# Kernel optimization log

Hardware: AMD Instinct MI355X
Metric: run time of the kernel (lower is better)

## Reference

```python
import jax, jax.numpy as jnp
import numpy as np


def _conv1x1(x, w, b):
    # x: [B,C,H,W], w: [O,C], b: [O] -> [B,O,H,W]
    return jnp.einsum('bchw,oc->bohw', x, w) + b[None, :, None, None]


def _maxpool2x2(x):
    # MaxPool2d(kernel_size=2, stride=2), VALID padding
    return jax.lax.reduce_window(
        x, -jnp.inf, jax.lax.max,
        window_dimensions=(1, 1, 2, 2),
        window_strides=(1, 1, 2, 2),
        padding='VALID')


def setup_inputs() -> dict:
    key = jax.random.key(0)
    ks = jax.random.split(key, 9)
    B, C, H, W = 8, 256, 64, 64
    c = 128  # in_channels // channel_scale_factor
    s = 0.05
    return {
        'x': jax.random.normal(ks[0], (B, C, H, W), jnp.float32),
        'theta_w': jax.random.normal(ks[1], (c, C), jnp.float32) * s,
        'theta_b': jax.random.normal(ks[2], (c,), jnp.float32) * s,
        'phi_w': jax.random.normal(ks[3], (c, C), jnp.float32) * s,
        'phi_b': jax.random.normal(ks[4], (c,), jnp.float32) * s,
        'g_w': jax.random.normal(ks[5], (c, C), jnp.float32) * s,
        'g_b': jax.random.normal(ks[6], (c,), jnp.float32) * s,
        'wz_w': jax.random.normal(ks[7], (C, c), jnp.float32) * s,
        'wz_b': jax.random.normal(ks[8], (C,), jnp.float32) * s,
    }


def reference(x, theta_w, theta_b, phi_w, phi_b, g_w, g_b, wz_w, wz_b):
    B, C, H, W = x.shape
    c = theta_w.shape[0]
    ox = x
    theta = _conv1x1(x, theta_w, theta_b)              # [B,c,H,W]
    xp = _maxpool2x2(x)                                # [B,C,h,w]
    phi = _conv1x1(xp, phi_w, phi_b)                   # [B,c,h,w]
    gi = _conv1x1(xp, g_w, g_b)                        # [B,c,h,w]

    N = H * W
    M = phi.shape[2] * phi.shape[3]
    theta1 = theta.reshape(B, c, N).transpose(0, 2, 1)  # [B,N,c]
    phi1 = phi.reshape(B, c, M)                         # [B,c,M]
    gi1 = gi.reshape(B, c, M).transpose(0, 2, 1)        # [B,M,c]

    m1 = jnp.einsum('bnc,bcm->bnm', theta1, phi1)       # [B,N,M] attention scores
    m1 = jax.nn.softmax(m1, axis=2)
    m2 = jnp.einsum('bnm,bmc->bnc', m1, gi1)            # [B,N,c]
    # Faithful to torch .view: raw-buffer reinterpretation, no transpose
    m3 = m2.reshape(B, c, H, W)
    m4 = _conv1x1(m3, wz_w, wz_b)                       # [B,C,H,W]
    return m4 + ox
```

## Files before the change

### kernel.cpp

```cpp
#include <hip/hip_runtime.h>
#include <math.h>

#define BATCH 8
#define CINCH 256
#define CMID  128
#define NPIX  4096
#define MPIX  1024

typedef __attribute__((ext_vector_type(8))) short bf16x8;
typedef __attribute__((ext_vector_type(4))) short s16x4;
typedef __attribute__((ext_vector_type(4))) float f32x4;

static __device__ __forceinline__ short f2bf(float f) {
    unsigned u = __float_as_uint(f);
    u = (u + 0x7fffu + ((u >> 16) & 1u)) >> 16;
    return (short)u;
}
static __device__ __forceinline__ float bf2f(short s) {
    return __uint_as_float(((unsigned)(unsigned short)s) << 16);
}

static __device__ __forceinline__ void gl16(const void* g, void* l) {
    __builtin_amdgcn_global_load_lds(
        (const __attribute__((address_space(1))) void*)g,
        (__attribute__((address_space(3))) void*)l, 16, 0, 0);
}

__global__ __launch_bounds__(256)
void wcvt_k(const float* __restrict__ a, const float* __restrict__ b,
            const float* __restrict__ c, const float* __restrict__ d,
            short* __restrict__ o)
{
    int i = (blockIdx.x * 256 + threadIdx.x) * 4;
    if (i < 32768) {
        int cr = i >> 8, col = i & 255;
        int R = (cr & 7) * 16 + (cr >> 3);
        float4 v = *(const float4*)(a + i);
        s16x4 rv = { f2bf(v.x * 1.44269504f), f2bf(v.y * 1.44269504f),
                     f2bf(v.z * 1.44269504f), f2bf(v.w * 1.44269504f) };
        *(s16x4*)(o + R * 256 + col) = rv;
    } else {
        const float* src; int j;
        if (i < 65536)      { src = b; j = i - 32768; }
        else if (i < 98304) { src = c; j = i - 65536; }
        else                { src = d; j = i - 98304; }
        float4 v = *(const float4*)(src + j);
        s16x4 rv = { f2bf(v.x), f2bf(v.y), f2bf(v.z), f2bf(v.w) };
        *(s16x4*)(o + i) = rv;
    }
}

__global__ __launch_bounds__(1024)
void front_k(const float* __restrict__ x,
             const short* __restrict__ th_wh, const float* __restrict__ th_b,
             const short* __restrict__ ph_wh, const float* __restrict__ ph_b,
             const short* __restrict__ g_wh,  const float* __restrict__ g_b,
             short* __restrict__ thetaO, short* __restrict__ phiO,
             short* __restrict__ gO)
{
    __shared__ float F[128 * 65];
    __shared__ short X[128 * 264];
    __shared__ short P[32 * 264];

    const int bid = blockIdx.x;
    const int t   = threadIdx.x;
    const int b   = bid & 7;
    const int r   = bid >> 3;
    const int wv  = t >> 6;
    const int l   = t & 63;
    const int lr  = l & 15;
    const int lg  = l >> 4;

    const int hh = wv & 1;
    const int c0 = wv >> 1;
    float ra[8], rb[8];
    {
        const float* xb = x + ((size_t)(b * 256)) * 4096 + r * 128;
#pragma unroll
        for (int i = 0; i < 8; ++i)
            ra[i] = xb[(size_t)(c0 + i * 8) * 4096 + hh * 64 + l];
    }
#pragma unroll
    for (int ct = 0; ct < 4; ++ct) {
        if ((ct & 1) == 0) {
#pragma unroll
            for (int i = 0; i < 8; ++i) F[(hh * 64 + l) * 65 + c0 + i * 8] = ra[i];
            if (ct < 3) {
                const float* xb = x + ((size_t)(b * 256 + (ct + 1) * 64)) * 4096 + r * 128;
#pragma unroll
                for (int i = 0; i < 8; ++i)
                    rb[i] = xb[(size_t)(c0 + i * 8) * 4096 + hh * 64 + l];
            }
        } else {
#pragma unroll
            for (int i = 0; i < 8; ++i) F[(hh * 64 + l) * 65 + c0 + i * 8] = rb[i];
            if (ct < 3) {
                const float* xb = x + ((size_t)(b * 256 + (ct + 1) * 64)) * 4096 + r * 128;
#pragma unroll
                for (int i = 0; i < 8; ++i)
                    ra[i] = xb[(size_t)(c0 + i * 8) * 4096 + hh * 64 + l];
            }
        }
        asm volatile("s_waitcnt lgkmcnt(0)" ::: "memory");
        __builtin_amdgcn_s_barrier();
#pragma unroll
        for (int i = 0; i < 8; ++i) {
            int slot = i * 1024 + t;
            int row = slot >> 6, ch = slot & 63;
            X[row * 264 + ct * 64 + ch] = f2bf(F[row * 65 + ch]);
        }
        asm volatile("s_waitcnt lgkmcnt(0)" ::: "memory");
        __builtin_amdgcn_s_barrier();
    }

#pragma unroll
    for (int i = 0; i < 2; ++i) {
        int slot = i * 1024 + t;
        int wp = slot >> 6, c4 = slot & 63;
        s16x4 v0 = *(const s16x4*)(X + (2 * wp) * 264 + c4 * 4);
        s16x4 v1 = *(const s16x4*)(X + (2 * wp + 1) * 264 + c4 * 4);
        s16x4 v2 = *(const s16x4*)(X + (64 + 2 * wp) * 264 + c4 * 4);
        s16x4 v3 = *(const s16x4*)(X + (65 + 2 * wp) * 264 + c4 * 4);
        s16x4 rm;
#pragma unroll
        for (int e = 0; e < 4; ++e) {
            float m = fmaxf(fmaxf(bf2f(v0[e]), bf2f(v1[e])),
                            fmaxf(bf2f(v2[e]), bf2f(v3[e])));
            rm[e] = f2bf(m);
        }
        *(s16x4*)(P + wp * 264 + c4 * 4) = rm;
    }
    __syncthreads();

    if (wv < 8) {
        const int m0 = wv * 16;
        f32x4 o[8];
#pragma unroll
        for (int dt = 0; dt < 8; ++dt)
#pragma unroll
            for (int e = 0; e < 4; ++e) o[dt][e] = 0.f;
        for (int kt = 0; kt < 8; ++kt) {
            bf16x8 a = *(const bf16x8*)(X + (m0 + lr) * 264 + kt * 32 + lg * 8);
#pragma unroll
            for (int dt = 0; dt < 8; ++dt) {
                bf16x8 bv = *(const bf16x8*)(th_wh + (size_t)(dt * 16 + lr) * 256 + kt * 32 + lg * 8);
                o[dt] = __builtin_amdgcn_mfma_f32_16x16x32_bf16(a, bv, o[dt], 0, 0, 0);
            }
        }
        float bvt[8];
#pragma unroll
        for (int dt = 0; dt < 8; ++dt) bvt[dt] = th_b[lr * 8 + dt] * 1.44269504f;
        short* ob = thetaO + (size_t)b * NPIX * 128;
#pragma unroll
        for (int rr = 0; rr < 4; ++rr) {
            int n = r * 128 + m0 + lg * 4 + rr;
            bf16x8 sv;
#pragma unroll
            for (int dt = 0; dt < 8; ++dt) sv[dt] = f2bf(o[dt][rr] + bvt[dt]);
            *(bf16x8*)(ob + (size_t)n * 128 + lr * 8) = sv;
        }
    } else {
        const int j    = wv & 3;
        const int half = j & 1;
        const int coH  = j >> 1;
        const bool isPhi = (wv < 12);
        const short* wsel = (isPhi ? ph_wh : g_wh) + (size_t)coH * 64 * 256;
        const float* bsel = isPhi ? ph_b : g_b;

        f32x4 q[4];
#pragma unroll
        for (int dt = 0; dt < 4; ++dt)
#pragma unroll
            for (int e = 0; e < 4; ++e) q[dt][e] = 0.f;
        for (int kt = 0; kt < 8; ++kt) {
            bf16x8 a = *(const bf16x8*)(P + (half * 16 + lr) * 264 + kt * 32 + lg * 8);
#pragma unroll
            for (int dt = 0; dt < 4; ++dt) {
                bf16x8 bv = *(const bf16x8*)(wsel + (size_t)(dt * 16 + lr) * 256 + kt * 32 + lg * 8);
                q[dt] = __builtin_amdgcn_mfma_f32_16x16x32_bf16(a, bv, q[dt], 0, 0, 0);
            }
        }
        float bv4[4];
#pragma unroll
        for (int dt = 0; dt < 4; ++dt) bv4[dt] = bsel[coH * 64 + dt * 16 + lr];

        if (isPhi) {
            short* cb = phiO + (size_t)b * 32 * 4096 + (size_t)r * 4096;
#pragma unroll
            for (int rr = 0; rr < 4; ++rr) {
                int mloc = half * 16 + lg * 4 + rr;
                short* cbb = cb + (mloc >> 4) * 512 + (mloc & 15) * 8;
#pragma unroll
                for (int dt = 0; dt < 4; ++dt) {
                    int cc = coH * 64 + dt * 16 + lr;
                    cbb[(cc >> 5) * 1024 + ((cc >> 3) & 3) * 128 + (cc & 7)]
                        = f2bf(q[dt][rr] + bv4[dt]);
                }
            }
        } else {
            short* cb = gO + (size_t)b * 32 * 4096 + (size_t)r * 4096;
            const int keyblk = half * 2 + (lg >> 1);
#pragma unroll
            for (int dt = 0; dt < 4; ++dt) {
                int cc = coH * 64 + dt * 16 + lr;
                s16x4 sv;
#pragma unroll
                for (int rr = 0; rr < 4; ++rr) sv[rr] = f2bf(q[dt][rr] + bv4[dt]);
                *(s16x4*)(cb + (size_t)((cc >> 4) * 64 + keyblk * 16 + (cc & 15)) * 8
                             + (lg & 1) * 4) = sv;
            }
        }
    }
}

__global__ __launch_bounds__(512)
void attn_fz(const short* __restrict__ theta, const short* __restrict__ phi_sw,
             const short* __restrict__ G_sw, const short* __restrict__ wzh,
             const float* __restrict__ wzb, const float* __restrict__ x,
             float* __restrict__ out)
{
    __shared__ __align__(16) char smem[147456];
    const int t   = threadIdx.x;
    const int wv  = t >> 6;
    const int l   = t & 63;
    const int lr  = l & 15;
    const int lg  = l >> 4;
    const int gid = wv >> 2;
    const int wvl = wv & 3;
    const int bid = blockIdx.x;
    const int b   = bid & 7;
    const int s   = bid >> 3;

    const short* thb = theta + (size_t)b * NPIX * 128;
    const char*  phC = (const char*)phi_sw + (size_t)b * 32 * 8192;
    const char*  gC  = (const char*)G_sw  + (size_t)b * 32 * 8192;
    const int first = gid * 16;

    auto STAGEP = [&](int bufi, int pi) {
#pragma unroll
        for (int sub = 0; sub < 2; ++sub) {
            int chunk = first + pi * 2 + sub;
            const char* ps = phC + (size_t)chunk * 8192 + wvl * 2048 + l * 16;
            const char* gs = gC  + (size_t)chunk * 8192 + wvl * 2048 + l * 16;
            char* base = smem + gid * 65536 + bufi * 32768 + sub * 16384;
            gl16(ps,        base + wvl * 2048);
            gl16(ps + 1024, base + wvl * 2048 + 1024);
            gl16(gs,        base + 8192 + wvl * 2048);
            gl16(gs + 1024, base + 8192 + wvl * 2048 + 1024);
        }
    };

    STAGEP(0, 0);

    bf16x8 bq[2][4];
#pragma unroll
    for (int u = 0; u < 2; ++u) {
        int n = ((wvl * 2 + u) * 16 + lr) * 32 + s;
#pragma unroll
        for (int kt = 0; kt < 4; ++kt)
            bq[u][kt] = *(const bf16x8*)(thb + (size_t)n * 128 + kt * 32 + lg * 8);
    }

    f32x4 o[2][8];
#pragma unroll
    for (int u = 0; u < 2; ++u)
#pragma unroll
        for (int dt = 0; dt < 8; ++dt)
#pragma unroll
            for (int e = 0; e < 4; ++e) o[u][dt][e] = 0.f;
    float ps_[2] = { 0.f, 0.f };

    for (int pi = 0; pi < 8; ++pi) {
        asm volatile("s_waitcnt vmcnt(0)" ::: "memory");
        __builtin_amdgcn_s_barrier();
        if (pi < 7) STAGEP((pi + 1) & 1, pi + 1);

#pragma unroll
        for (int sub = 0; sub < 2; ++sub) {
            const short* pb = (const short*)(smem + gid * 65536 + (pi & 1) * 32768
                                             + sub * 16384);
            const short* gb = pb + 4096;

            f32x4 ssw[2][2];
#pragma unroll
            for (int u = 0; u < 2; ++u)
#pragma unroll
                for (int mt = 0; mt < 2; ++mt)
#pragma unroll
                    for (int e = 0; e < 4; ++e) ssw[u][mt][e] = 0.f;
#pragma unroll
            for (int kt = 0; kt < 4; ++kt) {
                bf16x8 a0 = *(const bf16x8*)(pb + ((kt * 2 + 0) * 64 + l) * 8);
                bf16x8 a1 = *(const bf16x8*)(pb + ((kt * 2 + 1) * 64 + l) * 8);
#pragma unroll
                for (int u = 0; u < 2; ++u) {
                    ssw[u][0] = __builtin_amdgcn_mfma_f32_16x16x32_bf16(a0, bq[u][kt], ssw[u][0], 0, 0, 0);
                    ssw[u][1] = __builtin_amdgcn_mfma_f32_16x16x32_bf16(a1, bq[u][kt], ssw[u][1], 0, 0, 0);
                }
            }

            bf16x8 gf[8];
#pragma unroll
            for (int dt = 0; dt < 8; ++dt)
                gf[dt] = *(const bf16x8*)(gb + (dt * 64 + l) * 8);

#pragma unroll
            for (int u = 0; u < 2; ++u) {
                short* pu = (short*)(smem + 131072 + wv * 2048 + u * 1024);
#pragma unroll
                for (int mt = 0; mt < 2; ++mt) {
                    s16x4 pv;
#pragma unroll
                    for (int rr = 0; rr < 4; ++rr) {
                        float p = exp2f(ssw[u][mt][rr] - 40.f);
                        ps_[u] += p;
                        pv[rr] = f2bf(p);
                    }
                    *(s16x4*)(pu + ((mt * 2 + (lg >> 1)) * 16 + lr) * 8 + (lg & 1) * 4) = pv;
                }
                bf16x8 pa = *(const bf16x8*)(pu + l * 8);
#pragma unroll
                for (int dt = 0; dt < 8; ++dt)
                    o[u][dt] = __builtin_amdgcn_mfma_f32_16x16x32_bf16(pa, gf[dt], o[u][dt], 0, 0, 0);
            }
        }
    }

    const int co0 = wv * 32;
    bf16x8 afr[2][4];
#pragma unroll
    for (int nt = 0; nt < 2; ++nt) {
        int co = co0 + nt * 16 + lr;
#pragma unroll
        for (int kt = 0; kt < 4; ++kt)
            afr[nt][kt] = *(const bf16x8*)(wzh + (size_t)co * 128 + kt * 32 + lg * 8);
    }

    __syncthreads();
    float* mg = (float*)smem;
    short* m3l = (short*)(smem + 73728);
    if (wv >= 4) {
        float* mb = mg + (size_t)((wv - 4) * 64 + l) * 68;
#pragma unroll
        for (int u = 0; u < 2; ++u)
#pragma unroll
            for (int dt = 0; dt < 8; ++dt)
                *(f32x4*)(mb + (u * 8 + dt) * 4) = o[u][dt];
        mb[64] = ps_[0]; mb[65] = ps_[1];
    }
    __syncthreads();
    if (wv < 4) {
        const float* mb = mg + (size_t)(wv * 64 + l) * 68;
#pragma unroll
        for (int u = 0; u < 2; ++u)
#pragma unroll
            for (int dt = 0; dt < 8; ++dt) {
                f32x4 pv = *(const f32x4*)(mb + (u * 8 + dt) * 4);
#pragma unroll
                for (int e = 0; e < 4; ++e) o[u][dt][e] += pv[e];
            }
        ps_[0] += mb[64]; ps_[1] += mb[65];

#pragma unroll
        for (int u = 0; u < 2; ++u) {
            float tot = ps_[u];
            tot += __shfl_xor(tot, 16);
            tot += __shfl_xor(tot, 32);
            float inv = 1.f / tot;
            float invg[4];
#pragma unroll
            for (int rr = 0; rr < 4; ++rr) invg[rr] = __shfl(inv, lg * 4 + rr);
            const int cmb = (wvl * 2 + u) * 2 + (lg >> 1);
#pragma unroll
            for (int dt = 0; dt < 8; ++dt) {
                s16x4 zv;
#pragma unroll
                for (int rr = 0; rr < 4; ++rr) zv[rr] = f2bf(o[u][dt][rr] * invg[rr]);
                *(s16x4*)(m3l + (size_t)(cmb * 128 + dt * 16 + lr) * 8 + (lg & 1) * 4) = zv;
            }
        }
    }
    __syncthreads();

    {
        float xr[2][4][8];
#pragma unroll
        for (int nt = 0; nt < 2; ++nt)
#pragma unroll
            for (int rr = 0; rr < 4; ++rr) {
                int co = co0 + nt * 16 + lg * 4 + rr;
                const float* xb = x + ((size_t)b * 256 + co) * 4096 + s * 128;
#pragma unroll
                for (int dt = 0; dt < 8; ++dt)
                    xr[nt][rr][dt] = xb[dt * 16 + lr];
            }

        f32x4 oc[2][8];
#pragma unroll
        for (int nt = 0; nt < 2; ++nt)
#pragma unroll
            for (int dt = 0; dt < 8; ++dt)
#pragma unroll
                for (int e = 0; e < 4; ++e) oc[nt][dt][e] = 0.f;

#pragma unroll
        for (int dt = 0; dt < 8; ++dt) {
#pragma unroll
            for (int kt = 0; kt < 4; ++kt) {
                bf16x8 bz = *(const bf16x8*)(m3l + (size_t)((kt * 4 + lg) * 128 + dt * 16 + lr) * 8);
                oc[0][dt] = __builtin_amdgcn_mfma_f32_16x16x32_bf16(afr[0][kt], bz, oc[0][dt], 0, 0, 0);
                oc[1][dt] = __builtin_amdgcn_mfma_f32_16x16x32_bf16(afr[1][kt], bz, oc[1][dt], 0, 0, 0);
            }
        }

#pragma unroll
        for (int nt = 0; nt < 2; ++nt)
#pragma unroll
            for (int rr = 0; rr < 4; ++rr) {
                int co = co0 + nt * 16 + lg * 4 + rr;
                float bv = wzb[co];
                float* ob = out + ((size_t)b * 256 + co) * 4096 + s * 128;
#pragma unroll
                for (int dt = 0; dt < 8; ++dt) {
                    int lp = dt * 16 + lr;
                    ob[lp] = oc[nt][dt][rr] + bv + xr[nt][rr][dt];
                }
            }
    }
}

extern "C" void kernel_launch(void* const* d_in, const int* in_sizes, int n_in,
                              void* d_out, int out_size, void* d_ws, size_t ws_size,
                              hipStream_t stream)
{
    const float* x       = (const float*)d_in[0];
    const float* theta_w = (const float*)d_in[1];
    const float* theta_b = (const float*)d_in[2];
    const float* phi_w   = (const float*)d_in[3];
    const float* phi_b   = (const float*)d_in[4];
    const float* g_w     = (const float*)d_in[5];
    const float* g_b     = (const float*)d_in[6];
    const float* wz_w    = (const float*)d_in[7];
    const float* wz_b    = (const float*)d_in[8];
    float* out = (float*)d_out;

    short* ws      = (short*)d_ws;
    short* theta_h = ws;
    short* phi_h   = theta_h + (size_t)4194304;
    short* G_h     = phi_h + (size_t)1048576;
    short* wh      = G_h  + (size_t)1048576;
    short* th_wh = wh;
    short* ph_wh = wh + 32768;
    short* g_wh  = wh + 65536;
    short* wz_wh = wh + 98304;

    wcvt_k<<<dim3(128), 256, 0, stream>>>(theta_w, phi_w, g_w, wz_w, wh);

    front_k<<<dim3(256), 1024, 0, stream>>>(x, th_wh, theta_b, ph_wh, phi_b,
                                            g_wh, g_b, theta_h, phi_h, G_h);

    attn_fz<<<dim3(256), 512, 0, stream>>>(theta_h, phi_h, G_h,
                                           wz_wh, wz_b, x, out);
}
```

Measured before the change: 74.48 us.

## Double waves per attention block and use triple-buffered single-chunk staging

```diff
diff --git a/kernel.cpp b/kernel.cpp
--- a/kernel.cpp
+++ b/kernel.cpp
@@ -213,20 +213,20 @@
     }
 }
 
-__global__ __launch_bounds__(512)
+__global__ __launch_bounds__(1024, 4)
 void attn_fz(const short* __restrict__ theta, const short* __restrict__ phi_sw,
              const short* __restrict__ G_sw, const short* __restrict__ wzh,
              const float* __restrict__ wzb, const float* __restrict__ x,
              float* __restrict__ out)
 {
-    __shared__ __align__(16) char smem[147456];
+    __shared__ __align__(16) char smem[114688];
     const int t   = threadIdx.x;
     const int wv  = t >> 6;
     const int l   = t & 63;
     const int lr  = l & 15;
     const int lg  = l >> 4;
-    const int gid = wv >> 2;
-    const int wvl = wv & 3;
+    const int gid = wv >> 3;
+    const int wvl = wv & 7;
     const int bid = blockIdx.x;
     const int b   = bid & 7;
     const int s   = bid >> 3;
@@ -236,196 +236,160 @@
     const char*  gC  = (const char*)G_sw  + (size_t)b * 32 * 8192;
     const int first = gid * 16;
 
-    auto STAGEP = [&](int bufi, int pi) {
-#pragma unroll
-        for (int sub = 0; sub < 2; ++sub) {
-            int chunk = first + pi * 2 + sub;
-            const char* ps = phC + (size_t)chunk * 8192 + wvl * 2048 + l * 16;
-            const char* gs = gC  + (size_t)chunk * 8192 + wvl * 2048 + l * 16;
-            char* base = smem + gid * 65536 + bufi * 32768 + sub * 16384;
-            gl16(ps,        base + wvl * 2048);
-            gl16(ps + 1024, base + wvl * 2048 + 1024);
-            gl16(gs,        base + 8192 + wvl * 2048);
-            gl16(gs + 1024, base + 8192 + wvl * 2048 + 1024);
-        }
+    auto STAGE = [&](int bufi, int cc) {
+        int chunk = first + cc;
+        const char* ps = phC + (size_t)chunk * 8192 + wvl * 1024 + l * 16;
+        const char* gs = gC  + (size_t)chunk * 8192 + wvl * 1024 + l * 16;
+        char* base = smem + (gid * 3 + bufi) * 16384;
+        gl16(ps, base + wvl * 1024);
+        gl16(gs, base + 8192 + wvl * 1024);
     };
 
-    STAGEP(0, 0);
-
-    bf16x8 bq[2][4];
-#pragma unroll
-    for (int u = 0; u < 2; ++u) {
-        int n = ((wvl * 2 + u) * 16 + lr) * 32 + s;
+    STAGE(0, 0);
+    STAGE(1, 1);
+
+    bf16x8 bq[4];
+    {
+        int n = (wvl * 16 + lr) * 32 + s;
 #pragma unroll
         for (int kt = 0; kt < 4; ++kt)
-            bq[u][kt] = *(const bf16x8*)(thb + (size_t)n * 128 + kt * 32 + lg * 8);
-    }
-
-    f32x4 o[2][8];
-#pragma unroll
-    for (int u = 0; u < 2; ++u)
+            bq[kt] = *(const bf16x8*)(thb + (size_t)n * 128 + kt * 32 + lg * 8);
+    }
+
+    f32x4 o[8];
+#pragma unroll
+    for (int dt = 0; dt < 8; ++dt)
+#pragma unroll
+        for (int e = 0; e < 4; ++e) o[dt][e] = 0.f;
+    float ps_ = 0.f;
+
+    for (int c = 0; c < 16; ++c) {
+        if (c < 15) asm volatile("s_waitcnt vmcnt(2)" ::: "memory");
+        else        asm volatile("s_waitcnt vmcnt(0)" ::: "memory");
+        __builtin_amdgcn_s_barrier();
+        if (c < 14) STAGE((c + 2) % 3, c + 2);
+
+        const short* pb = (const short*)(smem + (gid * 3 + c % 3) * 16384);
+        const short* gb = pb + 4096;
+
+        f32x4 ssw[2];
+#pragma unroll
+        for (int mt = 0; mt < 2; ++mt)
+#pragma unroll
+            for (int e = 0; e < 4; ++e) ssw[mt][e] = 0.f;
+#pragma unroll
+        for (int kt = 0; kt < 4; ++kt) {
+            bf16x8 a0 = *(const bf16x8*)(pb + ((kt * 2 + 0) * 64 + l) * 8);
+            bf16x8 a1 = *(const bf16x8*)(pb + ((kt * 2 + 1) * 64 + l) * 8);
+            ssw[0] = __builtin_amdgcn_mfma_f32_16x16x32_bf16(a0, bq[kt], ssw[0], 0, 0, 0);
+            ssw[1] = __builtin_amdgcn_mfma_f32_16x16x32_bf16(a1, bq[kt], ssw[1], 0, 0, 0);
+        }
+
+        bf16x8 gf[8];
 #pragma unroll
         for (int dt = 0; dt < 8; ++dt)
-#pragma unroll
-            for (int e = 0; e < 4; ++e) o[u][dt][e] = 0.f;
-    float ps_[2] = { 0.f, 0.f };
-
-    for (int pi = 0; pi < 8; ++pi) {
-        asm volatile("s_waitcnt vmcnt(0)" ::: "memory");
-        __builtin_amdgcn_s_barrier();
-        if (pi < 7) STAGEP((pi + 1) & 1, pi + 1);
-
-#pragma unroll
-        for (int sub = 0; sub < 2; ++sub) {
-            const short* pb = (const short*)(smem + gid * 65536 + (pi & 1) * 32768
-                                             + sub * 16384);
-            const short* gb = pb + 4096;
-
-            f32x4 ssw[2][2];
-#pragma unroll
-            for (int u = 0; u < 2; ++u)
-#pragma unroll
-                for (int mt = 0; mt < 2; ++mt)
-#pragma unroll
-                    for (int e = 0; e < 4; ++e) ssw[u][mt][e] = 0.f;
-#pragma unroll
-            for (int kt = 0; kt < 4; ++kt) {
-                bf16x8 a0 = *(const bf16x8*)(pb + ((kt * 2 + 0) * 64 + l) * 8);
-                bf16x8 a1 = *(const bf16x8*)(pb + ((kt * 2 + 1) * 64 + l) * 8);
-#pragma unroll
-                for (int u = 0; u < 2; ++u) {
-                    ssw[u][0] = __builtin_amdgcn_mfma_f32_16x16x32_bf16(a0, bq[u][kt], ssw[u][0], 0, 0, 0);
-                    ssw[u][1] = __builtin_amdgcn_mfma_f32_16x16x32_bf16(a1, bq[u][kt], ssw[u][1], 0, 0, 0);
-                }
-            }
-
-            bf16x8 gf[8];
-#pragma unroll
-            for (int dt = 0; dt < 8; ++dt)
-                gf[dt] = *(const bf16x8*)(gb + (dt * 64 + l) * 8);
-
-#pragma unroll
-            for (int u = 0; u < 2; ++u) {
-                short* pu = (short*)(smem + 131072 + wv * 2048 + u * 1024);
-#pragma unroll
-                for (int mt = 0; mt < 2; ++mt) {
-                    s16x4 pv;
-#pragma unroll
-                    for (int rr = 0; rr < 4; ++rr) {
-                        float p = exp2f(ssw[u][mt][rr] - 40.f);
-                        ps_[u] += p;
-                        pv[rr] = f2bf(p);
-                    }
-                    *(s16x4*)(pu + ((mt * 2 + (lg >> 1)) * 16 + lr) * 8 + (lg & 1) * 4) = pv;
-                }
-                bf16x8 pa = *(const bf16x8*)(pu + l * 8);
-#pragma unroll
-                for (int dt = 0; dt < 8; ++dt)
-                    o[u][dt] = __builtin_amdgcn_mfma_f32_16x16x32_bf16(pa, gf[dt], o[u][dt], 0, 0, 0);
-            }
-        }
-    }
-
-    const int co0 = wv * 32;
-    bf16x8 afr[2][4];
-#pragma unroll
-    for (int nt = 0; nt < 2; ++nt) {
-        int co = co0 + nt * 16 + lr;
-#pragma unroll
-        for (int kt = 0; kt < 4; ++kt)
-            afr[nt][kt] = *(const bf16x8*)(wzh + (size_t)co * 128 + kt * 32 + lg * 8);
-    }
+            gf[dt] = *(const bf16x8*)(gb + (dt * 64 + l) * 8);
+
+        short* pu = (short*)(smem + 98304) + wv * 512;
+#pragma unroll
+        for (int mt = 0; mt < 2; ++mt) {
+            s16x4 pv;
+#pragma unroll
+            for (int rr = 0; rr < 4; ++rr) {
+                float p = exp2f(ssw[mt][rr] - 40.f);
+                ps_ += p;
+                pv[rr] = f2bf(p);
+            }
+            *(s16x4*)(pu + ((mt * 2 + (lg >> 1)) * 16 + lr) * 8 + (lg & 1) * 4) = pv;
+        }
+        bf16x8 pa = *(const bf16x8*)(pu + l * 8);
+#pragma unroll
+        for (int dt = 0; dt < 8; ++dt)
+            o[dt] = __builtin_amdgcn_mfma_f32_16x16x32_bf16(pa, gf[dt], o[dt], 0, 0, 0);
+    }
+
+    const int co0 = wv * 16;
+    bf16x8 afr[4];
+#pragma unroll
+    for (int kt = 0; kt < 4; ++kt)
+        afr[kt] = *(const bf16x8*)(wzh + (size_t)(co0 + lr) * 128 + kt * 32 + lg * 8);
 
     __syncthreads();
     float* mg = (float*)smem;
     short* m3l = (short*)(smem + 73728);
-    if (wv >= 4) {
-        float* mb = mg + (size_t)((wv - 4) * 64 + l) * 68;
-#pragma unroll
-        for (int u = 0; u < 2; ++u)
+    if (wv >= 8) {
+        float* mb = mg + (size_t)((wv - 8) * 64 + l) * 33;
+#pragma unroll
+        for (int dt = 0; dt < 8; ++dt)
+            *(f32x4*)(mb + dt * 4) = o[dt];
+        mb[32] = ps_;
+    }
+    __syncthreads();
+    if (wv < 8) {
+        const float* mb = mg + (size_t)(wv * 64 + l) * 33;
+#pragma unroll
+        for (int dt = 0; dt < 8; ++dt) {
+            f32x4 pv = *(const f32x4*)(mb + dt * 4);
+#pragma unroll
+            for (int e = 0; e < 4; ++e) o[dt][e] += pv[e];
+        }
+        ps_ += mb[32];
+
+        float tot = ps_;
+        tot += __shfl_xor(tot, 16);
+        tot += __shfl_xor(tot, 32);
+        float inv = 1.f / tot;
+        float invg[4];
+#pragma unroll
+        for (int rr = 0; rr < 4; ++rr) invg[rr] = __shfl(inv, lg * 4 + rr);
+        const int cmb = wvl * 2 + (lg >> 1);
+#pragma unroll
+        for (int dt = 0; dt < 8; ++dt) {
+            s16x4 zv;
+#pragma unroll
+            for (int rr = 0; rr < 4; ++rr) zv[rr] = f2bf(o[dt][rr] * invg[rr]);
+            *(s16x4*)(m3l + (size_t)(cmb * 128 + dt * 16 + lr) * 8 + (lg & 1) * 4) = zv;
+        }
+    }
+    __syncthreads();
+
+    {
+        float xr[4][8];
+#pragma unroll
+        for (int rr = 0; rr < 4; ++rr) {
+            int co = co0 + lg * 4 + rr;
+            const float* xb = x + ((size_t)b * 256 + co) * 4096 + s * 128;
 #pragma unroll
             for (int dt = 0; dt < 8; ++dt)
-                *(f32x4*)(mb + (u * 8 + dt) * 4) = o[u][dt];
-        mb[64] = ps_[0]; mb[65] = ps_[1];
-    }
-    __syncthreads();
-    if (wv < 4) {
-        const float* mb = mg + (size_t)(wv * 64 + l) * 68;
-#pragma unroll
-        for (int u = 0; u < 2; ++u)
-#pragma unroll
-            for (int dt = 0; dt < 8; ++dt) {
-                f32x4 pv = *(const f32x4*)(mb + (u * 8 + dt) * 4);
-#pragma unroll
-                for (int e = 0; e < 4; ++e) o[u][dt][e] += pv[e];
-            }
-        ps_[0] += mb[64]; ps_[1] += mb[65];
-
-#pragma unroll
-        for (int u = 0; u < 2; ++u) {
-            float tot = ps_[u];
-            tot += __shfl_xor(tot, 16);
-            tot += __shfl_xor(tot, 32);
-            float inv = 1.f / tot;
-            float invg[4];
-#pragma unroll
-            for (int rr = 0; rr < 4; ++rr) invg[rr] = __shfl(inv, lg * 4 + rr);
-            const int cmb = (wvl * 2 + u) * 2 + (lg >> 1);
-#pragma unroll
-            for (int dt = 0; dt < 8; ++dt) {
-                s16x4 zv;
-#pragma unroll
-                for (int rr = 0; rr < 4; ++rr) zv[rr] = f2bf(o[u][dt][rr] * invg[rr]);
-                *(s16x4*)(m3l + (size_t)(cmb * 128 + dt * 16 + lr) * 8 + (lg & 1) * 4) = zv;
-            }
-        }
-    }
-    __syncthreads();
-
-    {
-        float xr[2][4][8];
-#pragma unroll
-        for (int nt = 0; nt < 2; ++nt)
-#pragma unroll
-            for (int rr = 0; rr < 4; ++rr) {
-                int co = co0 + nt * 16 + lg * 4 + rr;
-                const float* xb = x + ((size_t)b * 256 + co) * 4096 + s * 128;
-#pragma unroll
-                for (int dt = 0; dt < 8; ++dt)
-                    xr[nt][rr][dt] = xb[dt * 16 + lr];
-            }
-
-        f32x4 oc[2][8];
-#pragma unroll
-        for (int nt = 0; nt < 2; ++nt)
-#pragma unroll
-            for (int dt = 0; dt < 8; ++dt)
-#pragma unroll
-                for (int e = 0; e < 4; ++e) oc[nt][dt][e] = 0.f;
+                xr[rr][dt] = xb[dt * 16 + lr];
+        }
+
+        f32x4 oc[8];
+#pragma unroll
+        for (int dt = 0; dt < 8; ++dt)
+#pragma unroll
+            for (int e = 0; e < 4; ++e) oc[dt][e] = 0.f;
 
 #pragma unroll
         for (int dt = 0; dt < 8; ++dt) {
 #pragma unroll
             for (int kt = 0; kt < 4; ++kt) {
                 bf16x8 bz = *(const bf16x8*)(m3l + (size_t)((kt * 4 + lg) * 128 + dt * 16 + lr) * 8);
-                oc[0][dt] = __builtin_amdgcn_mfma_f32_16x16x32_bf16(afr[0][kt], bz, oc[0][dt], 0, 0, 0);
-                oc[1][dt] = __builtin_amdgcn_mfma_f32_16x16x32_bf16(afr[1][kt], bz, oc[1][dt], 0, 0, 0);
-            }
-        }
-
-#pragma unroll
-        for (int nt = 0; nt < 2; ++nt)
-#pragma unroll
-            for (int rr = 0; rr < 4; ++rr) {
-                int co = co0 + nt * 16 + lg * 4 + rr;
-                float bv = wzb[co];
-                float* ob = out + ((size_t)b * 256 + co) * 4096 + s * 128;
-#pragma unroll
-                for (int dt = 0; dt < 8; ++dt) {
-                    int lp = dt * 16 + lr;
-                    ob[lp] = oc[nt][dt][rr] + bv + xr[nt][rr][dt];
-                }
-            }
+                oc[dt] = __builtin_amdgcn_mfma_f32_16x16x32_bf16(afr[kt], bz, oc[dt], 0, 0, 0);
+            }
+        }
+
+#pragma unroll
+        for (int rr = 0; rr < 4; ++rr) {
+            int co = co0 + lg * 4 + rr;
+            float bv = wzb[co];
+            float* ob = out + ((size_t)b * 256 + co) * 4096 + s * 128;
+#pragma unroll
+            for (int dt = 0; dt < 8; ++dt) {
+                int lp = dt * 16 + lr;
+                ob[lp] = oc[dt][rr] + bv + xr[rr][dt];
+            }
+        }
     }
 }
 
@@ -459,6 +423,6 @@
     front_k<<<dim3(256), 1024, 0, stream>>>(x, th_wh, theta_b, ph_wh, phi_b,
                                             g_wh, g_b, theta_h, phi_h, G_h);
 
-    attn_fz<<<dim3(256), 512, 0, stream>>>(theta_h, phi_h, G_h,
-                                           wz_wh, wz_b, x, out);
-}
+    attn_fz<<<dim3(256), 1024, 0, stream>>>(theta_h, phi_h, G_h,
+                                            wz_wh, wz_b, x, out);
+}
```

Result: slower. 77.50 us (+4.0%).
